# Kernel tuning notes

Hardware: AMD Instinct MI355X
Metric: run time of the kernel (lower is better)

## Reference

```python
import jax, jax.numpy as jnp
import numpy as np

B, S, DIN, DSLOT, NHEADS = 1024, 1024, 128, 64, 2
TEMPERATURE = 1.0


def setup_inputs() -> dict:
    key = jax.random.key(0)
    ks = jax.random.split(key, 7)
    slot_feats = jax.random.normal(ks[0], (B, S, DIN), dtype=jnp.float32)
    slot_mask = jax.random.uniform(ks[1], (B, S), dtype=jnp.float32)
    # slot_mlp: Linear(DIN, DSLOT) -> ReLU -> Linear(DSLOT, DSLOT)
    W1 = jax.random.normal(ks[2], (DIN, DSLOT), dtype=jnp.float32) * (1.0 / np.sqrt(DIN))
    b1 = jnp.zeros((DSLOT,), dtype=jnp.float32)
    W2 = jax.random.normal(ks[3], (DSLOT, DSLOT), dtype=jnp.float32) * (1.0 / np.sqrt(DSLOT))
    b2 = jnp.zeros((DSLOT,), dtype=jnp.float32)
    q = jax.random.normal(ks[4], (NHEADS, DSLOT), dtype=jnp.float32) * 0.1
    return {"slot_feats": slot_feats, "slot_mask": slot_mask,
            "W1": W1, "b1": b1, "W2": W2, "b2": b2, "q": q, "k": 8}


def reference(slot_feats, slot_mask, W1, b1, W2, b2, q, k):
    d_slot = W2.shape[-1]
    # slot MLP embed: [B,S,Dslot]
    H = jnp.maximum(slot_feats @ W1 + b1, 0.0) @ W2 + b2
    scale = 1.0 / jnp.sqrt(jnp.asarray(d_slot, dtype=H.dtype))
    # per-head score, averaged over heads: [B,S]
    scores = jnp.einsum('bsd,hd->bsh', H, q).mean(axis=-1) * scale
    mask = slot_mask > 0.5
    scores_masked = jnp.where(mask, scores, -jnp.inf)
    all_masked = ~jnp.any(mask, axis=1)  # [B]
    temp = max(TEMPERATURE, 1e-6)
    sm_in = jnp.where(all_masked[:, None], jnp.zeros_like(scores), scores_masked) / temp
    attnW = jax.nn.softmax(sm_in, axis=1)  # [B,S]
    ctx = jnp.einsum('bs,bsd->bd', attnW, H)  # use_soft_ctx=True
    # top-k on raw masked scores (eval: no gumbel)
    k_eff = min(k, scores.shape[1])
    invalid_rows = jnp.all(jnp.isinf(scores_masked), axis=1)
    safe_scores = jnp.where(invalid_rows[:, None], jnp.zeros_like(scores_masked), scores_masked)
    _, topk_idx = jax.lax.top_k(safe_scores, k_eff)  # [B,k]
    sel = jnp.take_along_axis(H, topk_idx[:, :, None], axis=1)  # [B,k,Dslot]
    return sel, ctx, attnW
```

## Files before the change

kernel.cpp:

```cpp
#include <hip/hip_runtime.h>
#include <hip/hip_bf16.h>

#define BB 1024
#define SS 1024
#define DIN 128
#define DSLOT 64
#define TOPK 8
#define TOKENS (BB*SS)
#define TM 128

__device__ __forceinline__ unsigned short f2bf(float x) {
    unsigned u = __float_as_uint(x);
    return (unsigned short)((u + 0x7fffu + ((u >> 16) & 1u)) >> 16);
}
__device__ __forceinline__ float bf2f(unsigned u16) {
    return __uint_as_float(u16 << 16);
}

__global__ void prep_kernel(const float* __restrict__ W2, const float* __restrict__ b2,
                            const float* __restrict__ q, float* __restrict__ vv) {
    __shared__ float qm[64];
    int d = threadIdx.x;
    if (d < 64) qm[d] = (q[d] + q[64 + d]) * 0.0625f;
    __syncthreads();
    if (d < 64) {
        float acc = 0.f;
        #pragma unroll
        for (int j = 0; j < 64; ++j) acc = fmaf(W2[d * 64 + j], qm[j], acc);
        vv[d] = acc;
    }
    if (d == 0) {
        float c = 0.f;
        for (int j = 0; j < 64; ++j) c = fmaf(b2[j], qm[j], c);
        vv[64] = c;
    }
}

__global__ __launch_bounds__(256) void mlp_kernel(
    const float* __restrict__ feats, const float* __restrict__ W1,
    const float* __restrict__ b1, const float* __restrict__ W2,
    const float* __restrict__ b2, const float* __restrict__ vv,
    unsigned short* __restrict__ Hws, float* __restrict__ scores)
{
    __shared__ float Xs[TM][33];
    __shared__ unsigned short Hs[TM][66];
    __shared__ float W1s[32][64];
    __shared__ float W2s[64][64];
    __shared__ float vS[64], b1s[64], b2s[64];
    __shared__ float c0s;

    const int tid = threadIdx.x;
    const int tx = tid & 3;
    const int ty = tid >> 2;
    const int d0 = tx * 16;
    const long t0 = (long)blockIdx.x * TM;

    for (int i = tid; i < 64 * 64; i += 256) W2s[i >> 6][i & 63] = W2[i];
    if (tid < 64) { vS[tid] = vv[tid]; b1s[tid] = b1[tid]; b2s[tid] = b2[tid]; }
    if (tid == 0) c0s = vv[64];

    float acc1[2][16];
    #pragma unroll
    for (int t = 0; t < 2; ++t)
        #pragma unroll
        for (int j = 0; j < 16; ++j) acc1[t][j] = 0.f;

    for (int kc = 0; kc < 4; ++kc) {
        __syncthreads();
        #pragma unroll
        for (int i = 0; i < 4; ++i) {
            int li = tid + i * 256;
            int row = li >> 3, c4 = li & 7;
            float4 f = *(const float4*)&feats[(t0 + row) * DIN + kc * 32 + c4 * 4];
            Xs[row][c4 * 4 + 0] = f.x; Xs[row][c4 * 4 + 1] = f.y;
            Xs[row][c4 * 4 + 2] = f.z; Xs[row][c4 * 4 + 3] = f.w;
        }
        #pragma unroll
        for (int i = 0; i < 2; ++i) {
            int li = tid + i * 256;
            int row = li >> 4, c4 = li & 15;
            *(float4*)&W1s[row][c4 * 4] = *(const float4*)&W1[(kc * 32 + row) * DSLOT + c4 * 4];
        }
        __syncthreads();
        #pragma unroll 8
        for (int kk = 0; kk < 32; ++kk) {
            float w[16];
            *(float4*)&w[0]  = *(const float4*)&W1s[kk][d0];
            *(float4*)&w[4]  = *(const float4*)&W1s[kk][d0 + 4];
            *(float4*)&w[8]  = *(const float4*)&W1s[kk][d0 + 8];
            *(float4*)&w[12] = *(const float4*)&W1s[kk][d0 + 12];
            float x0 = Xs[2 * ty + 0][kk];
            float x1 = Xs[2 * ty + 1][kk];
            #pragma unroll
            for (int j = 0; j < 16; ++j) {
                acc1[0][j] = fmaf(x0, w[j], acc1[0][j]);
                acc1[1][j] = fmaf(x1, w[j], acc1[1][j]);
            }
        }
    }

    float h[2][16];
    #pragma unroll
    for (int t = 0; t < 2; ++t)
        #pragma unroll
        for (int j = 0; j < 16; ++j) h[t][j] = fmaxf(acc1[t][j] + b1s[d0 + j], 0.f);

    float p0 = 0.f, p1 = 0.f;
    #pragma unroll
    for (int j = 0; j < 16; ++j) {
        p0 = fmaf(h[0][j], vS[d0 + j], p0);
        p1 = fmaf(h[1][j], vS[d0 + j], p1);
    }
    p0 += __shfl_xor(p0, 1); p0 += __shfl_xor(p0, 2);
    p1 += __shfl_xor(p1, 1); p1 += __shfl_xor(p1, 2);
    if (tx == 0) {
        scores[t0 + 2 * ty + 0] = p0 + c0s;
        scores[t0 + 2 * ty + 1] = p1 + c0s;
    }

    #pragma unroll
    for (int t = 0; t < 2; ++t)
        #pragma unroll
        for (int j = 0; j < 8; ++j) {
            unsigned pk = (unsigned)f2bf(h[t][2 * j]) | ((unsigned)f2bf(h[t][2 * j + 1]) << 16);
            *(unsigned*)&Hs[2 * ty + t][d0 + 2 * j] = pk;
        }
    __syncthreads();

    float acc2[2][16];
    #pragma unroll
    for (int t = 0; t < 2; ++t)
        #pragma unroll
        for (int j = 0; j < 16; ++j) acc2[t][j] = b2s[d0 + j];

    #pragma unroll 8
    for (int kk = 0; kk < 64; ++kk) {
        float w[16];
        *(float4*)&w[0]  = *(const float4*)&W2s[kk][d0];
        *(float4*)&w[4]  = *(const float4*)&W2s[kk][d0 + 4];
        *(float4*)&w[8]  = *(const float4*)&W2s[kk][d0 + 8];
        *(float4*)&w[12] = *(const float4*)&W2s[kk][d0 + 12];
        float x0 = bf2f(Hs[2 * ty + 0][kk]);
        float x1 = bf2f(Hs[2 * ty + 1][kk]);
        #pragma unroll
        for (int j = 0; j < 16; ++j) {
            acc2[0][j] = fmaf(x0, w[j], acc2[0][j]);
            acc2[1][j] = fmaf(x1, w[j], acc2[1][j]);
        }
    }

    #pragma unroll
    for (int t = 0; t < 2; ++t) {
        unsigned hw[8];
        #pragma unroll
        for (int j = 0; j < 8; ++j)
            hw[j] = (unsigned)f2bf(acc2[t][2 * j]) | ((unsigned)f2bf(acc2[t][2 * j + 1]) << 16);
        unsigned* dst = (unsigned*)&Hws[(t0 + 2 * ty + t) * DSLOT + d0];
        *(uint4*)dst = make_uint4(hw[0], hw[1], hw[2], hw[3]);
        *((uint4*)dst + 1) = make_uint4(hw[4], hw[5], hw[6], hw[7]);
    }
}

__global__ __launch_bounds__(256) void attn_kernel(
    const float* __restrict__ scores, const float* __restrict__ mask,
    const unsigned short* __restrict__ Hws,
    float* __restrict__ out_sel, float* __restrict__ out_ctx, float* __restrict__ out_attn)
{
    const int b = blockIdx.x, tid = threadIdx.x;
    __shared__ float sc[SS];
    __shared__ float ex[SS];
    __shared__ float red[256];
    __shared__ int   redi[256];
    __shared__ unsigned char used[SS];
    __shared__ int anyValid;
    __shared__ int selIdx[TOPK];

    if (tid == 0) anyValid = 0;
    __syncthreads();

    const float* srow = scores + (long)b * SS;
    const float* mrow = mask + (long)b * SS;
    int localAny = 0;
    #pragma unroll
    for (int k = 0; k < 4; ++k) {
        int i = tid + k * 256;
        bool valid = mrow[i] > 0.5f;
        sc[i] = valid ? srow[i] : -__builtin_inff();
        used[i] = 0;
        if (valid) localAny = 1;
    }
    if (localAny) atomicOr(&anyValid, 1);
    __syncthreads();
    const int av = anyValid;

    float mloc = -__builtin_inff();
    #pragma unroll
    for (int k = 0; k < 4; ++k) {
        int i = tid + k * 256;
        mloc = fmaxf(mloc, av ? sc[i] : 0.f);
    }
    red[tid] = mloc; __syncthreads();
    for (int s = 128; s > 0; s >>= 1) {
        if (tid < s) red[tid] = fmaxf(red[tid], red[tid + s]);
        __syncthreads();
    }
    const float M = red[0];
    __syncthreads();

    float sloc = 0.f;
    #pragma unroll
    for (int k = 0; k < 4; ++k) {
        int i = tid + k * 256;
        float v = av ? sc[i] : 0.f;
        float e = expf(v - M);
        ex[i] = e; sloc += e;
    }
    red[tid] = sloc; __syncthreads();
    for (int s = 128; s > 0; s >>= 1) {
        if (tid < s) red[tid] += red[tid + s];
        __syncthreads();
    }
    const float invZ = 1.f / red[0];
    __syncthreads();
    #pragma unroll
    for (int k = 0; k < 4; ++k) {
        int i = tid + k * 256;
        float w = ex[i] * invZ;
        ex[i] = w;
        out_attn[(long)b * SS + i] = w;
    }

    for (int r = 0; r < TOPK; ++r) {
        float bv = -__builtin_inff(); int bi = SS;
        #pragma unroll
        for (int k = 0; k < 4; ++k) {
            int i = tid + k * 256;
            if (!used[i]) {
                float v = av ? sc[i] : 0.f;
                if (v > bv || (v == bv && i < bi)) { bv = v; bi = i; }
            }
        }
        red[tid] = bv; redi[tid] = bi; __syncthreads();
        for (int s = 128; s > 0; s >>= 1) {
            if (tid < s) {
                float v2 = red[tid + s]; int i2 = redi[tid + s];
                if (v2 > red[tid] || (v2 == red[tid] && i2 < redi[tid])) {
                    red[tid] = v2; redi[tid] = i2;
                }
            }
            __syncthreads();
        }
        if (tid == 0) { selIdx[r] = redi[0]; used[redi[0]] = 1; }
        __syncthreads();
    }

    for (int f = tid; f < TOPK * DSLOT; f += 256) {
        int r = f >> 6, d = f & 63;
        unsigned short hb = Hws[((long)b * SS + selIdx[r]) * DSLOT + d];
        out_sel[(long)b * (TOPK * DSLOT) + f] = bf2f(hb);
    }

    const int dg = tid & 15, sg = tid >> 4;
    float a0 = 0.f, a1 = 0.f, a2 = 0.f, a3 = 0.f;
    #pragma unroll 4
    for (int it = 0; it < 64; ++it) {
        int s = sg * 64 + it;
        uint2 u = *(const uint2*)&Hws[((long)b * SS + s) * DSLOT + dg * 4];
        float w = ex[s];
        a0 = fmaf(w, bf2f(u.x & 0xffffu), a0);
        a1 = fmaf(w, bf2f(u.x >> 16), a1);
        a2 = fmaf(w, bf2f(u.y & 0xffffu), a2);
        a3 = fmaf(w, bf2f(u.y >> 16), a3);
    }
    __syncthreads();
    sc[sg * 64 + dg * 4 + 0] = a0;
    sc[sg * 64 + dg * 4 + 1] = a1;
    sc[sg * 64 + dg * 4 + 2] = a2;
    sc[sg * 64 + dg * 4 + 3] = a3;
    __syncthreads();
    if (tid < 64) {
        float acc = 0.f;
        #pragma unroll
        for (int g = 0; g < 16; ++g) acc += sc[g * 64 + tid];
        out_ctx[(long)b * DSLOT + tid] = acc;
    }
}

extern "C" void kernel_launch(void* const* d_in, const int* in_sizes, int n_in,
                              void* d_out, int out_size, void* d_ws, size_t ws_size,
                              hipStream_t stream) {
    (void)in_sizes; (void)n_in; (void)out_size; (void)ws_size;
    const float* feats = (const float*)d_in[0];
    const float* smask = (const float*)d_in[1];
    const float* W1 = (const float*)d_in[2];
    const float* b1 = (const float*)d_in[3];
    const float* W2 = (const float*)d_in[4];
    const float* b2 = (const float*)d_in[5];
    const float* q  = (const float*)d_in[6];

    char* ws = (char*)d_ws;
    unsigned short* Hws = (unsigned short*)ws;
    float* scores = (float*)(ws + (size_t)TOKENS * DSLOT * 2);
    float* vv = (float*)(ws + (size_t)TOKENS * DSLOT * 2 + (size_t)TOKENS * 4);

    float* out_sel  = (float*)d_out;
    float* out_ctx  = out_sel + (long)BB * TOPK * DSLOT;
    float* out_attn = out_ctx + (long)BB * DSLOT;

    prep_kernel<<<1, 64, 0, stream>>>(W2, b2, q, vv);
    mlp_kernel<<<TOKENS / TM, 256, 0, stream>>>(feats, W1, b1, W2, b2, vv, Hws, scores);
    attn_kernel<<<BB, 256, 0, stream>>>(scores, smask, Hws, out_sel, out_ctx, out_attn);
}
```

Baseline: 1.020 ms.

## Defer second linear layer to after attention using linearity of ctx and selection

The MLP kernel now stores only the ReLU hidden layer, dropping the per-token second matmul. The attention kernel applies W2 and b2 to the selected top-k rows and to the softmax-weighted context, which works because softmax weights sum to one. This removes a 64x64 matmul per token, shrinking the MLP kernel's shared memory, and adds a launch-bounds occupancy hint. The softmax and top-k reductions switch from shared-memory tree loops to wave shuffles. Rounding changes, since the context is now formed from bf16 hidden activations before W2 rather than from bf16 outputs.

```diff
diff --git a/kernel.cpp b/kernel.cpp
--- a/kernel.cpp
+++ b/kernel.cpp
@@ -36,17 +36,14 @@
     }
 }
 
-__global__ __launch_bounds__(256) void mlp_kernel(
+__global__ __launch_bounds__(256, 5) void mlp_kernel(
     const float* __restrict__ feats, const float* __restrict__ W1,
-    const float* __restrict__ b1, const float* __restrict__ W2,
-    const float* __restrict__ b2, const float* __restrict__ vv,
-    unsigned short* __restrict__ Hws, float* __restrict__ scores)
+    const float* __restrict__ b1, const float* __restrict__ vv,
+    unsigned short* __restrict__ hws, float* __restrict__ scores)
 {
     __shared__ float Xs[TM][33];
-    __shared__ unsigned short Hs[TM][66];
     __shared__ float W1s[32][64];
-    __shared__ float W2s[64][64];
-    __shared__ float vS[64], b1s[64], b2s[64];
+    __shared__ float vS[64], b1s[64];
     __shared__ float c0s;
 
     const int tid = threadIdx.x;
@@ -55,8 +52,7 @@
     const int d0 = tx * 16;
     const long t0 = (long)blockIdx.x * TM;
 
-    for (int i = tid; i < 64 * 64; i += 256) W2s[i >> 6][i & 63] = W2[i];
-    if (tid < 64) { vS[tid] = vv[tid]; b1s[tid] = b1[tid]; b2s[tid] = b2[tid]; }
+    if (tid < 64) { vS[tid] = vv[tid]; b1s[tid] = b1[tid]; }
     if (tid == 0) c0s = vv[64];
 
     float acc1[2][16];
@@ -119,43 +115,12 @@
     }
 
     #pragma unroll
-    for (int t = 0; t < 2; ++t)
-        #pragma unroll
-        for (int j = 0; j < 8; ++j) {
-            unsigned pk = (unsigned)f2bf(h[t][2 * j]) | ((unsigned)f2bf(h[t][2 * j + 1]) << 16);
-            *(unsigned*)&Hs[2 * ty + t][d0 + 2 * j] = pk;
-        }
-    __syncthreads();
-
-    float acc2[2][16];
-    #pragma unroll
-    for (int t = 0; t < 2; ++t)
-        #pragma unroll
-        for (int j = 0; j < 16; ++j) acc2[t][j] = b2s[d0 + j];
-
-    #pragma unroll 8
-    for (int kk = 0; kk < 64; ++kk) {
-        float w[16];
-        *(float4*)&w[0]  = *(const float4*)&W2s[kk][d0];
-        *(float4*)&w[4]  = *(const float4*)&W2s[kk][d0 + 4];
-        *(float4*)&w[8]  = *(const float4*)&W2s[kk][d0 + 8];
-        *(float4*)&w[12] = *(const float4*)&W2s[kk][d0 + 12];
-        float x0 = bf2f(Hs[2 * ty + 0][kk]);
-        float x1 = bf2f(Hs[2 * ty + 1][kk]);
-        #pragma unroll
-        for (int j = 0; j < 16; ++j) {
-            acc2[0][j] = fmaf(x0, w[j], acc2[0][j]);
-            acc2[1][j] = fmaf(x1, w[j], acc2[1][j]);
-        }
-    }
-
-    #pragma unroll
     for (int t = 0; t < 2; ++t) {
         unsigned hw[8];
         #pragma unroll
         for (int j = 0; j < 8; ++j)
-            hw[j] = (unsigned)f2bf(acc2[t][2 * j]) | ((unsigned)f2bf(acc2[t][2 * j + 1]) << 16);
-        unsigned* dst = (unsigned*)&Hws[(t0 + 2 * ty + t) * DSLOT + d0];
+            hw[j] = (unsigned)f2bf(h[t][2 * j]) | ((unsigned)f2bf(h[t][2 * j + 1]) << 16);
+        unsigned* dst = (unsigned*)&hws[(t0 + 2 * ty + t) * DSLOT + d0];
         *(uint4*)dst = make_uint4(hw[0], hw[1], hw[2], hw[3]);
         *((uint4*)dst + 1) = make_uint4(hw[4], hw[5], hw[6], hw[7]);
     }
@@ -163,125 +128,143 @@
 
 __global__ __launch_bounds__(256) void attn_kernel(
     const float* __restrict__ scores, const float* __restrict__ mask,
-    const unsigned short* __restrict__ Hws,
+    const unsigned short* __restrict__ hws,
+    const float* __restrict__ W2, const float* __restrict__ b2,
     float* __restrict__ out_sel, float* __restrict__ out_ctx, float* __restrict__ out_attn)
 {
     const int b = blockIdx.x, tid = threadIdx.x;
-    __shared__ float sc[SS];
+    const int lane = tid & 63, wv = tid >> 6;
+
     __shared__ float ex[SS];
-    __shared__ float red[256];
-    __shared__ int   redi[256];
-    __shared__ unsigned char used[SS];
-    __shared__ int anyValid;
-    __shared__ int selIdx[TOPK];
-
-    if (tid == 0) anyValid = 0;
+    __shared__ float W2s[64][64];
+    __shared__ float b2s[64];
+    __shared__ float hselF[TOPK][64];
+    __shared__ float cpart[16][65];
+    __shared__ float ctxh[64];
+    __shared__ float wredA[4], wredB[4];
+    __shared__ float rv[4];
+    __shared__ int   ri[4];
+    __shared__ int   selIdx[TOPK];
+    __shared__ int   anyv;
+
+    for (int i = tid; i < 64 * 64; i += 256) W2s[i >> 6][i & 63] = W2[i];
+    if (tid < 64) b2s[tid] = b2[tid];
+    if (tid == 0) anyv = 0;
     __syncthreads();
 
     const float* srow = scores + (long)b * SS;
     const float* mrow = mask + (long)b * SS;
+
+    float tv[4];
     int localAny = 0;
     #pragma unroll
     for (int k = 0; k < 4; ++k) {
         int i = tid + k * 256;
         bool valid = mrow[i] > 0.5f;
-        sc[i] = valid ? srow[i] : -__builtin_inff();
-        used[i] = 0;
+        tv[k] = valid ? srow[i] : -__builtin_inff();
         if (valid) localAny = 1;
     }
-    if (localAny) atomicOr(&anyValid, 1);
-    __syncthreads();
-    const int av = anyValid;
-
-    float mloc = -__builtin_inff();
+    if (localAny) atomicOr(&anyv, 1);
+    __syncthreads();
+    const int av = anyv;
+    if (!av) { tv[0] = 0.f; tv[1] = 0.f; tv[2] = 0.f; tv[3] = 0.f; }
+
+    float m = fmaxf(fmaxf(tv[0], tv[1]), fmaxf(tv[2], tv[3]));
+    #pragma unroll
+    for (int off = 32; off > 0; off >>= 1) m = fmaxf(m, __shfl_xor(m, off));
+    if (lane == 0) wredA[wv] = m;
+    __syncthreads();
+    const float M = fmaxf(fmaxf(wredA[0], wredA[1]), fmaxf(wredA[2], wredA[3]));
+
+    float e[4];
+    float s = 0.f;
+    #pragma unroll
+    for (int k = 0; k < 4; ++k) { e[k] = expf(tv[k] - M); s += e[k]; }
+    #pragma unroll
+    for (int off = 32; off > 0; off >>= 1) s += __shfl_xor(s, off);
+    if (lane == 0) wredB[wv] = s;
+    __syncthreads();
+    const float invZ = 1.f / (wredB[0] + wredB[1] + wredB[2] + wredB[3]);
     #pragma unroll
     for (int k = 0; k < 4; ++k) {
         int i = tid + k * 256;
-        mloc = fmaxf(mloc, av ? sc[i] : 0.f);
-    }
-    red[tid] = mloc; __syncthreads();
-    for (int s = 128; s > 0; s >>= 1) {
-        if (tid < s) red[tid] = fmaxf(red[tid], red[tid + s]);
-        __syncthreads();
-    }
-    const float M = red[0];
-    __syncthreads();
-
-    float sloc = 0.f;
-    #pragma unroll
-    for (int k = 0; k < 4; ++k) {
-        int i = tid + k * 256;
-        float v = av ? sc[i] : 0.f;
-        float e = expf(v - M);
-        ex[i] = e; sloc += e;
-    }
-    red[tid] = sloc; __syncthreads();
-    for (int s = 128; s > 0; s >>= 1) {
-        if (tid < s) red[tid] += red[tid + s];
-        __syncthreads();
-    }
-    const float invZ = 1.f / red[0];
-    __syncthreads();
-    #pragma unroll
-    for (int k = 0; k < 4; ++k) {
-        int i = tid + k * 256;
-        float w = ex[i] * invZ;
+        float w = e[k] * invZ;
         ex[i] = w;
         out_attn[(long)b * SS + i] = w;
     }
 
+    unsigned usedm = 0;
     for (int r = 0; r < TOPK; ++r) {
-        float bv = -__builtin_inff(); int bi = SS;
+        float bv = -__builtin_inff(); int bi = 0x7fffffff;
         #pragma unroll
         for (int k = 0; k < 4; ++k) {
-            int i = tid + k * 256;
-            if (!used[i]) {
-                float v = av ? sc[i] : 0.f;
+            if (!(usedm & (1u << k))) {
+                float v = tv[k]; int i = tid + k * 256;
                 if (v > bv || (v == bv && i < bi)) { bv = v; bi = i; }
             }
         }
-        red[tid] = bv; redi[tid] = bi; __syncthreads();
-        for (int s = 128; s > 0; s >>= 1) {
-            if (tid < s) {
-                float v2 = red[tid + s]; int i2 = redi[tid + s];
-                if (v2 > red[tid] || (v2 == red[tid] && i2 < redi[tid])) {
-                    red[tid] = v2; redi[tid] = i2;
-                }
-            }
-            __syncthreads();
-        }
-        if (tid == 0) { selIdx[r] = redi[0]; used[redi[0]] = 1; }
-        __syncthreads();
-    }
-
-    for (int f = tid; f < TOPK * DSLOT; f += 256) {
+        #pragma unroll
+        for (int off = 32; off > 0; off >>= 1) {
+            float ov = __shfl_xor(bv, off); int oi = __shfl_xor(bi, off);
+            if (ov > bv || (ov == bv && oi < bi)) { bv = ov; bi = oi; }
+        }
+        if (lane == 0) { rv[wv] = bv; ri[wv] = bi; }
+        __syncthreads();
+        float cv = rv[0]; int ci = ri[0];
+        #pragma unroll
+        for (int w = 1; w < 4; ++w) {
+            if (rv[w] > cv || (rv[w] == cv && ri[w] < ci)) { cv = rv[w]; ci = ri[w]; }
+        }
+        if (tid == 0) selIdx[r] = ci;
+        if ((ci & 255) == tid) usedm |= 1u << (ci >> 8);
+        __syncthreads();
+    }
+
+    {
+        int r = tid >> 5, cp = tid & 31;
+        unsigned u = *(const unsigned*)&hws[((long)b * SS + selIdx[r]) * DSLOT + cp * 2];
+        hselF[r][cp * 2 + 0] = bf2f(u & 0xffffu);
+        hselF[r][cp * 2 + 1] = bf2f(u >> 16);
+    }
+    __syncthreads();
+    #pragma unroll
+    for (int o = 0; o < 2; ++o) {
+        int f = tid + o * 256;
         int r = f >> 6, d = f & 63;
-        unsigned short hb = Hws[((long)b * SS + selIdx[r]) * DSLOT + d];
-        out_sel[(long)b * (TOPK * DSLOT) + f] = bf2f(hb);
+        float acc = b2s[d];
+        #pragma unroll
+        for (int j = 0; j < 64; ++j) acc = fmaf(hselF[r][j], W2s[j][d], acc);
+        out_sel[(long)b * (TOPK * DSLOT) + f] = acc;
     }
 
     const int dg = tid & 15, sg = tid >> 4;
     float a0 = 0.f, a1 = 0.f, a2 = 0.f, a3 = 0.f;
     #pragma unroll 4
     for (int it = 0; it < 64; ++it) {
-        int s = sg * 64 + it;
-        uint2 u = *(const uint2*)&Hws[((long)b * SS + s) * DSLOT + dg * 4];
-        float w = ex[s];
+        int ss = sg * 64 + it;
+        uint2 u = *(const uint2*)&hws[((long)b * SS + ss) * DSLOT + dg * 4];
+        float w = ex[ss];
         a0 = fmaf(w, bf2f(u.x & 0xffffu), a0);
         a1 = fmaf(w, bf2f(u.x >> 16), a1);
         a2 = fmaf(w, bf2f(u.y & 0xffffu), a2);
         a3 = fmaf(w, bf2f(u.y >> 16), a3);
     }
-    __syncthreads();
-    sc[sg * 64 + dg * 4 + 0] = a0;
-    sc[sg * 64 + dg * 4 + 1] = a1;
-    sc[sg * 64 + dg * 4 + 2] = a2;
-    sc[sg * 64 + dg * 4 + 3] = a3;
+    cpart[sg][dg * 4 + 0] = a0;
+    cpart[sg][dg * 4 + 1] = a1;
+    cpart[sg][dg * 4 + 2] = a2;
+    cpart[sg][dg * 4 + 3] = a3;
     __syncthreads();
     if (tid < 64) {
         float acc = 0.f;
         #pragma unroll
-        for (int g = 0; g < 16; ++g) acc += sc[g * 64 + tid];
+        for (int g = 0; g < 16; ++g) acc += cpart[g][tid];
+        ctxh[tid] = acc;
+    }
+    __syncthreads();
+    if (tid < 64) {
+        float acc = b2s[tid];
+        #pragma unroll
+        for (int j = 0; j < 64; ++j) acc = fmaf(ctxh[j], W2s[j][tid], acc);
         out_ctx[(long)b * DSLOT + tid] = acc;
     }
 }
@@ -299,7 +282,7 @@
     const float* q  = (const float*)d_in[6];
 
     char* ws = (char*)d_ws;
-    unsigned short* Hws = (unsigned short*)ws;
+    unsigned short* hws = (unsigned short*)ws;
     float* scores = (float*)(ws + (size_t)TOKENS * DSLOT * 2);
     float* vv = (float*)(ws + (size_t)TOKENS * DSLOT * 2 + (size_t)TOKENS * 4);
 
@@ -308,6 +291,6 @@
     float* out_attn = out_ctx + (long)BB * DSLOT;
 
     prep_kernel<<<1, 64, 0, stream>>>(W2, b2, q, vv);
-    mlp_kernel<<<TOKENS / TM, 256, 0, stream>>>(feats, W1, b1, W2, b2, vv, Hws, scores);
-    attn_kernel<<<BB, 256, 0, stream>>>(scores, smask, Hws, out_sel, out_ctx, out_attn);
-}
+    mlp_kernel<<<TOKENS / TM, 256, 0, stream>>>(feats, W1, b1, vv, hws, scores);
+    attn_kernel<<<BB, 256, 0, stream>>>(scores, smask, hws, W2, b2, out_sel, out_ctx, out_attn);
+}
```

Result: faster. 879.2 us (-13.8%).
